# Kernel optimization log

Hardware: AMD Instinct MI355X
Metric: run time of the kernel (lower is better)

Reference implementation:

```python
import jax, jax.numpy as jnp
import numpy as np

B, S, D = 4, 2048, 1024
H = 16
HD = D // H  # head_dim = 64


def setup_inputs() -> dict:
    key = jax.random.key(0)
    ks = jax.random.split(key, 5)
    scale = 1.0 / np.sqrt(D)
    return {
        "x": jax.random.normal(ks[0], (B, S, D), dtype=jnp.float32),
        "Wq": jax.random.normal(ks[1], (D, D), dtype=jnp.float32) * scale,
        "Wk": jax.random.normal(ks[2], (D, D), dtype=jnp.float32) * scale,
        "Wv": jax.random.normal(ks[3], (D, D), dtype=jnp.float32) * scale,
        "Wo": jax.random.normal(ks[4], (D, D), dtype=jnp.float32) * scale,
        "bo": jnp.zeros((D,), dtype=jnp.float32),
    }


def reference(x, Wq, Wk, Wv, Wo, bo):
    b, s, d = x.shape
    # project and split heads: [b, h, s, hd]
    q = (x @ Wq).reshape(b, s, H, HD).transpose(0, 2, 1, 3)
    k = (x @ Wk).reshape(b, s, H, HD).transpose(0, 2, 1, 3)
    v = (x @ Wv).reshape(b, s, H, HD).transpose(0, 2, 1, 3)
    # scores: [b, h, s, s]
    scores = jnp.einsum("bhqd,bhkd->bhqk", q, k)
    # NOTE: original uses tril(diagonal=1) -> allows one future token (off-by-one)
    mask = jnp.tril(jnp.ones((s, s), dtype=bool), k=1)
    scores = jnp.where(mask, scores, -jnp.inf)
    attn = jax.nn.softmax(scores / np.sqrt(HD), axis=-1)
    # dropout p=0.0 (deterministic baseline): identity
    ctx = jnp.einsum("bhqk,bhkd->bhqd", attn, v)
    ctx = ctx.transpose(0, 2, 1, 3).reshape(b, s, d)
    return ctx @ Wo + bo
```

## Files before the change

### kernel.cpp

```cpp
#include <hip/hip_runtime.h>
#include <hip/hip_bf16.h>

#define Bq 4
#define Sq 2048
#define Dq 1024
#define Hq 16
#define HDq 64
#define Mq (Bq*Sq)

typedef unsigned short u16;
typedef __attribute__((ext_vector_type(8))) __bf16 b16x8;
typedef __attribute__((ext_vector_type(4))) float f32x4;
typedef __attribute__((ext_vector_type(4))) unsigned int u32x4;

__device__ inline float bf2f(u16 h){ union{unsigned u; float f;} v; v.u = ((unsigned)h)<<16; return v.f; }
__device__ inline u16 f2bf(float f){ union{float f; unsigned u;} v; v.f=f; unsigned r = v.u + 0x7FFFu + ((v.u>>16)&1u); return (u16)(r>>16); }
__device__ inline u16 truncbf(float f){ union{float f; unsigned u;} v; v.f=f; return (u16)(v.u>>16); }
__device__ inline float ld_elem(const void* p, size_t i, int isf32){
  return isf32 ? ((const float*)p)[i] : bf2f(((const u16*)p)[i]);
}
__device__ inline void ld16(const u16* g, u16* l){
  __builtin_amdgcn_global_load_lds((const __attribute__((address_space(1))) void*)g,
                                   (__attribute__((address_space(3))) void*)l, 16, 0, 0);
}

#if __has_builtin(__builtin_amdgcn_exp2f)
#define EXP2(x) __builtin_amdgcn_exp2f(x)
#else
#define EXP2(x) __expf((x)*0.69314718056f)
#endif
#define SCALE_LOG2E 0.18033688011112042f

__global__ void detect_dtype(const unsigned* __restrict__ x, int* __restrict__ flag){
  __shared__ int cnt;
  if(threadIdx.x==0) cnt=0;
  __syncthreads();
  int local=0;
  for(int i=threadIdx.x;i<2048;i+=256){
    unsigned w = x[i];
    if(((w>>7)&0xFFu)>=0x90u) local++;
    if(((w>>23)&0xFFu)>=0x90u) local++;
  }
  atomicAdd(&cnt, local);
  __syncthreads();
  if(threadIdx.x==0) *flag = (cnt>64) ? 1 : 0;
}

__global__ __launch_bounds__(256) void convert_x(const void* __restrict__ x, u16* __restrict__ xc,
                                                 const int* __restrict__ flag, int n){
  const int f = *flag;
  int i = (blockIdx.x*256 + threadIdx.x)*8;
  if(i>=n) return;
  if(f){
    const float* xf=(const float*)x;
    #pragma unroll
    for(int j=0;j<8;j++) xc[i+j] = f2bf(xf[i+j]);
  } else {
    *(u32x4*)&xc[i] = *(const u32x4*)((const u16*)x + i);
  }
}

__global__ __launch_bounds__(256) void transpose_w(
    const void* __restrict__ W0, const void* __restrict__ W1,
    const void* __restrict__ W2, const void* __restrict__ W3,
    u16* __restrict__ T0, u16* __restrict__ T1,
    u16* __restrict__ T2, u16* __restrict__ T3,
    const int* __restrict__ flag){
  __shared__ u16 tile[64][65];
  const int f = *flag;
  const int z = blockIdx.z;
  const void* src = (z==0)?W0:(z==1)?W1:(z==2)?W2:W3;
  u16*       dst = (z==0)?T0:(z==1)?T1:(z==2)?T2:T3;
  const int t = threadIdx.x;
  const int k0 = blockIdx.x*64, n0 = blockIdx.y*64;
  #pragma unroll
  for(int r=0;r<16;r++){
    int row = r*4 + (t>>6), col = t&63;
    tile[row][col] = f2bf(ld_elem(src, (size_t)(k0+row)*Dq + n0 + col, f));
  }
  __syncthreads();
  #pragma unroll
  for(int r=0;r<16;r++){
    int row = r*4 + (t>>6), col = t&63;
    dst[(size_t)(n0+row)*Dq + k0 + col] = tile[col][row];
  }
}

__global__ __launch_bounds__(256) void gemm_bf0(
    const u16* __restrict__ A, const u16* __restrict__ Bt,
    u16* __restrict__ O0, u16* __restrict__ O1, u16* __restrict__ O2){
  constexpr int NT = Dq/32;
  __shared__ u16 Apriv[2][4][2048];
  __shared__ u16 Bpriv[2][4][2048];
  const int t = threadIdx.x;
  const int lane = t & 63, wave = t >> 6;
  const int quad = lane >> 4, l16 = lane & 15;
  const int wr = wave >> 1, wc = wave & 1;
  int L = blockIdx.x + blockIdx.y*gridDim.x;
  int k8 = L & 7, ii = L >> 3;
  int nsb = ii >> 6, rem = ii & 63;
  int mg = rem >> 3, ng = rem & 7;
  const int m0 = (k8*8 + mg)*128, n0 = (nsb*8 + ng)*128;

  f32x4 acc[4][4] = {};

  auto stage = [&](int T, int s){
    const int k0 = T<<5;
    #pragma unroll
    for(int r=0;r<4;r++){
      int idx = lane + (r<<6);
      int row = idx>>2, g = idx&3;
      int gl = g ^ ((row>>1)&3);
      ld16(&A[(size_t)(m0 + wr*64 + row)*Dq + k0 + gl*8], &Apriv[s][wave][idx*8]);
    }
    #pragma unroll
    for(int r=0;r<4;r++){
      int idx = lane + (r<<6);
      int row = idx>>2, g = idx&3;
      int gl = g ^ ((row>>1)&3);
      ld16(&Bt[(size_t)(n0 + wc*64 + row)*Dq + k0 + gl*8], &Bpriv[s][wave][idx*8]);
    }
  };
  auto ldA = [&](int s, int i)->b16x8{
    int row = i*16 + l16;
    return *(const b16x8*)&Apriv[s][wave][row*32 + ((quad ^ ((row>>1)&3))<<3)];
  };
  auto ldB = [&](int s, int j)->b16x8{
    int row = j*16 + l16;
    return *(const b16x8*)&Bpriv[s][wave][row*32 + ((quad ^ ((row>>1)&3))<<3)];
  };
  #define MFMA_BF16 __builtin_amdgcn_mfma_f32_16x16x32_bf16

  stage(0, 0);

  for(int tt=0; tt<NT; ++tt){
    const int s = tt&1;
    if(tt+1<NT){
      stage(tt+1, s^1);
      asm volatile("s_waitcnt vmcnt(8)" ::: "memory");
    } else {
      asm volatile("s_waitcnt vmcnt(0)" ::: "memory");
    }
    __builtin_amdgcn_sched_barrier(0);
    b16x8 af[4], bf[4];
    #pragma unroll
    for(int i=0;i<4;i++) af[i]=ldA(s,i);
    #pragma unroll
    for(int j=0;j<4;j++) bf[j]=ldB(s,j);
    asm volatile("s_waitcnt lgkmcnt(0)" ::: "memory");
    __builtin_amdgcn_sched_barrier(0);
    __builtin_amdgcn_s_setprio(1);
    #pragma unroll
    for(int i=0;i<4;i++)
      #pragma unroll
      for(int j=0;j<4;j++)
        acc[i][j]=MFMA_BF16(af[i],bf[j],acc[i][j],0,0,0);
    __builtin_amdgcn_s_setprio(0);
  }

  #pragma unroll
  for(int i=0;i<4;i++){
    #pragma unroll
    for(int j=0;j<4;j++){
      int n = n0 + wc*64 + j*16 + l16;
      #pragma unroll
      for(int r=0;r<4;r++){
        int m = m0 + wr*64 + i*16 + quad*4 + r;
        float c = acc[i][j][r];
        int z = n >> 10, nn2 = n & 1023;
        int b = m >> 11, s2 = m & 2047;
        int h = nn2 >> 6, hd = nn2 & 63;
        if (z==0)      O0[(((size_t)(b*Hq + h))*Sq + s2)*HDq + hd] = f2bf(c*SCALE_LOG2E);
        else if (z==1) O1[(((size_t)(b*Hq + h))*Sq + s2)*HDq + hd] = f2bf(c);
        else           O2[(((size_t)(b*Hq + h))*HDq + hd)*Sq + s2] = f2bf(c);
      }
    }
  }
  #undef MFMA_BF16
}

__global__ __launch_bounds__(256, 3) void gemm_op(
    const u16* __restrict__ A, const u16* __restrict__ Bt,
    void* __restrict__ Og, const void* __restrict__ bias, const int* __restrict__ flag){
  constexpr int NT = Dq/32;
  __shared__ u16 Asl[3][128*32];
  __shared__ u16 Bsl[3][128*32];
  const int f = *flag;
  const int t = threadIdx.x;
  const int lane = t & 63, wave = t >> 6;
  const int quad = lane >> 4, l16 = lane & 15;
  const int wr = wave >> 1, wc = wave & 1;
  int L = blockIdx.x + blockIdx.y*gridDim.x;
  int k8 = L & 7, ii = L >> 3;
  int mg = ii >> 3, ng = ii & 7;
  const int m0 = (k8*8 + mg)*128, n0 = ng*128;

  f32x4 acc[4][4] = {};

  auto stageA = [&](int T, int s){
    #pragma unroll
    for(int r=0;r<2;r++){
      int idx = t + (r<<8);
      int row = idx>>2, g = idx&3;
      int gl = g ^ ((row>>1)&3);
      ld16(&A[(size_t)(m0+row)*Dq + (T<<5) + gl*8], &Asl[s][idx*8]);
    }
  };
  auto stageB = [&](int T, int s){
    #pragma unroll
    for(int r=0;r<2;r++){
      int idx = t + (r<<8);
      int row = idx>>2, g = idx&3;
      int gl = g ^ ((row>>1)&3);
      ld16(&Bt[(size_t)(n0+row)*Dq + (T<<5) + gl*8], &Bsl[s][idx*8]);
    }
  };
  auto ldA = [&](int s, int i)->b16x8{
    int row = wr*64 + i*16 + l16;
    return *(const b16x8*)&Asl[s][row*32 + ((quad ^ ((row>>1)&3))<<3)];
  };
  auto ldB = [&](int s, int j)->b16x8{
    int row = wc*64 + j*16 + l16;
    return *(const b16x8*)&Bsl[s][row*32 + ((quad ^ ((row>>1)&3))<<3)];
  };
  #define MFMA_BF16 __builtin_amdgcn_mfma_f32_16x16x32_bf16

  stageA(0,0); stageB(0,0); stageA(1,1); stageB(1,1);
  asm volatile("s_waitcnt vmcnt(4)" ::: "memory");
  __builtin_amdgcn_s_barrier();
  __builtin_amdgcn_sched_barrier(0);

  int s0=0, s1=1, s2=2;
  for(int tt=0; tt<NT; ++tt){
    if(tt+2<NT){ stageA(tt+2, s2); stageB(tt+2, s2); }
    b16x8 af[4], bf[4];
    #pragma unroll
    for(int i=0;i<4;i++) af[i]=ldA(s0,i);
    #pragma unroll
    for(int j=0;j<4;j++) bf[j]=ldB(s0,j);
    __builtin_amdgcn_s_barrier();
    asm volatile("s_waitcnt lgkmcnt(0)" ::: "memory");
    __builtin_amdgcn_sched_barrier(0);
    __builtin_amdgcn_s_setprio(1);
    #pragma unroll
    for(int i=0;i<4;i++)
      #pragma unroll
      for(int j=0;j<4;j++)
        acc[i][j]=MFMA_BF16(af[i],bf[j],acc[i][j],0,0,0);
    __builtin_amdgcn_s_setprio(0);
    if(tt<NT-2) asm volatile("s_waitcnt vmcnt(4)" ::: "memory");
    else        asm volatile("s_waitcnt vmcnt(0)" ::: "memory");
    __builtin_amdgcn_s_barrier();
    __builtin_amdgcn_sched_barrier(0);
    int x=s0; s0=s1; s1=s2; s2=x;
  }

  #pragma unroll
  for(int i=0;i<4;i++){
    #pragma unroll
    for(int j=0;j<4;j++){
      int n = n0 + wc*64 + j*16 + l16;
      #pragma unroll
      for(int r=0;r<4;r++){
        int m = m0 + wr*64 + i*16 + quad*4 + r;
        float c2 = acc[i][j][r] + ld_elem(bias, n, f);
        if (f) ((float*)Og)[(size_t)m*Dq + n] = c2;
        else   ((u16*)Og)[(size_t)m*Dq + n]   = f2bf(c2);
      }
    }
  }
  #undef MFMA_BF16
}

__global__ __launch_bounds__(256) void flash_attn(
    const u16* __restrict__ Q, const u16* __restrict__ K,
    const u16* __restrict__ VT, u16* __restrict__ C){
  __shared__ u16 Kt[128*64];
  __shared__ u16 Vt[64*128];
  __shared__ u16 Pl[4][16][72];
  const int t = threadIdx.x;
  const int lane = t&63, wave = t>>6, quad = lane>>4, l16 = lane&15;
  int L  = blockIdx.x + blockIdx.y*gridDim.x;
  int k8 = L & 7, ii = L >> 3;
  const int bh = k8*8 + (ii>>4);
  const int p  = ii & 15;
  const int b = bh >> 4, h = bh & 15;
  const int qt[2] = { p, 31 - p };
  int nk[2];
  #pragma unroll
  for(int tt=0;tt<2;tt++){ int v = qt[tt]+2; nk[tt] = (v<32)?v:32; }
  const int nrounds = (nk[1]+1)>>1;
  const u16* Qh = Q  + (size_t)bh*Sq*HDq;
  const u16* Kh = K  + (size_t)bh*Sq*HDq;
  const u16* Vh = VT + (size_t)bh*HDq*Sq;

  b16x8 aq[2][2];
  #pragma unroll
  for(int tt=0;tt<2;tt++){
    const u16* qp = Qh + (size_t)(qt[tt]*64 + wave*16 + l16)*HDq + quad*8;
    aq[tt][0] = *(const b16x8*)qp;
    aq[tt][1] = *(const b16x8*)(qp + 32);
  }
  b16x8 vone;
  #pragma unroll
  for(int i=0;i<8;i++) vone[i] = (__bf16)1.0f;

  const f32x4 fzero = {0.f,0.f,0.f,0.f};
  f32x4 Oa[2][4]; f32x4 lacc[2];
  #pragma unroll
  for(int tt=0;tt<2;tt++){ lacc[tt]=fzero; for(int j=0;j<4;j++) Oa[tt][j]=fzero; }

  for(int kt2=0; kt2<nrounds; kt2++){
    __syncthreads();
    #pragma unroll
    for(int r=0;r<4;r++){
      int idx = t + (r<<8);
      int row = idx>>3, g = idx&7;
      int csw = (g ^ (row&7))<<3;
      ld16(Kh + (size_t)(kt2*128+row)*HDq + csw, Kt + idx*8);
    }
    #pragma unroll
    for(int r=0;r<4;r++){
      int idx = t + (r<<8);
      int row = idx>>4, g = idx&15;
      int csw = (g ^ (row&15))<<3;
      ld16(Vh + (size_t)row*Sq + (size_t)kt2*128 + csw, Vt + idx*8);
    }
    __syncthreads();

    #pragma unroll
    for(int half=0; half<2; half++){
      const int kt = kt2*2 + half;
      #pragma unroll
      for(int tt=0;tt<2;tt++){
        if (kt >= nk[tt]) continue;
        const int qq0 = qt[tt]*64;
        f32x4 sc[4];
        #pragma unroll
        for(int jn=0;jn<4;jn++){
          int krow = half*64 + jn*16 + l16;
          const u16* kp = &Kt[krow*64];
          f32x4 s = fzero;
          b16x8 bk0 = *(const b16x8*)&kp[((quad     ^ (krow&7))<<3)];
          b16x8 bk1 = *(const b16x8*)&kp[(((quad+4) ^ (krow&7))<<3)];
          s = __builtin_amdgcn_mfma_f32_16x16x32_bf16(aq[tt][0], bk0, s, 0,0,0);
          s = __builtin_amdgcn_mfma_f32_16x16x32_bf16(aq[tt][1], bk1, s, 0,0,0);
          sc[jn] = s;
        }
        if (kt < qt[tt]) {
          #pragma unroll
          for(int jn=0;jn<4;jn++)
            #pragma unroll
            for(int r=0;r<4;r++)
              Pl[wave][quad*4+r][jn*16+l16] = truncbf(EXP2(sc[jn][r]));
        } else {
          const int qbase = qq0 + wave*16 + quad*4;
          #pragma unroll
          for(int jn=0;jn<4;jn++){
            int kg = kt*64 + jn*16 + l16;
            #pragma unroll
            for(int r=0;r<4;r++){
              float sv = sc[jn][r];
              if (kg > qbase + r + 1) sv = -__builtin_inff();
              Pl[wave][quad*4+r][jn*16+l16] = truncbf(EXP2(sv));
            }
          }
        }
        #pragma unroll
        for(int ks=0;ks<2;ks++){
          b16x8 ap = *(const b16x8*)&Pl[wave][l16][ks*32 + quad*8];
          int glog = half*8 + ks*4 + quad;
          #pragma unroll
          for(int jd=0;jd<4;jd++){
            int hd = jd*16 + l16;
            b16x8 bv = *(const b16x8*)&Vt[hd*128 + ((glog ^ (hd&15))<<3)];
            Oa[tt][jd] = __builtin_amdgcn_mfma_f32_16x16x32_bf16(ap, bv, Oa[tt][jd], 0,0,0);
          }
          lacc[tt] = __builtin_amdgcn_mfma_f32_16x16x32_bf16(ap, vone, lacc[tt], 0,0,0);
        }
      }
    }
  }
  #pragma unroll
  for(int tt=0;tt<2;tt++){
    const int qq0 = qt[tt]*64;
    #pragma unroll
    for(int r=0;r<4;r++){
      int s = qq0 + wave*16 + quad*4 + r;
      float inv = 1.0f / lacc[tt][r];
      #pragma unroll
      for(int jd=0;jd<4;jd++)
        C[((size_t)(b*Sq + s))*Dq + h*HDq + jd*16 + l16] = f2bf(Oa[tt][jd][r]*inv);
    }
  }
}

extern "C" void kernel_launch(void* const* d_in, const int* in_sizes, int n_in,
                              void* d_out, int out_size, void* d_ws, size_t ws_size,
                              hipStream_t stream){
  const void* x  = d_in[0];
  const void* Wq = d_in[1];
  const void* Wk = d_in[2];
  const void* Wv = d_in[3];
  const void* Wo = d_in[4];
  const void* bo = d_in[5];

  char* ws = (char*)d_ws;
  size_t off = 0;
  auto wsalloc = [&](size_t bytes)->void*{
    void* p = ws + off; off += (bytes + 255) & ~(size_t)255; return p;
  };
  int* flag = (int*)wsalloc(256);
  u16* WqT = (u16*)wsalloc((size_t)Dq*Dq*2);
  u16* WkT = (u16*)wsalloc((size_t)Dq*Dq*2);
  u16* WvT = (u16*)wsalloc((size_t)Dq*Dq*2);
  u16* WoT = (u16*)wsalloc((size_t)Dq*Dq*2);
  u16* xc  = (u16*)wsalloc((size_t)Mq*Dq*2);
  u16* Qb  = (u16*)wsalloc((size_t)Mq*Dq*2);
  u16* Kb  = (u16*)wsalloc((size_t)Mq*Dq*2);
  u16* VTb = (u16*)wsalloc((size_t)Mq*Dq*2);
  u16* Cb  = (u16*)wsalloc((size_t)Mq*Dq*2);

  detect_dtype<<<1, 256, 0, stream>>>((const unsigned*)x, flag);
  convert_x<<<dim3(Mq*Dq/8/256), 256, 0, stream>>>(x, xc, flag, Mq*Dq);
  transpose_w<<<dim3(16,16,4), 256, 0, stream>>>(Wq,Wk,Wv,Wo, WqT,WkT,WvT,WoT, flag);
  gemm_bf0<<<dim3(24, 64), 256, 0, stream>>>(xc, WqT, Qb,Kb,VTb);
  flash_attn<<<dim3(16, Bq*Hq), 256, 0, stream>>>(Qb, Kb, VTb, Cb);
  gemm_op<<<dim3(8, 64), 256, 0, stream>>>(Cb, WoT, d_out, bo, flag);
}
```

Before: 226.1 us.

## Fuse prep kernels with in-wave dtype detection; QKV GEMM loads A into registers

Merges dtype detection, x conversion and weight transposition into one prep kernel. Each wave now detects the dtype with a ballot over a sample of x, which removes the flag buffer and two launches. The QKV GEMM is restructured so A fragments are loaded straight from global memory into registers and double-buffered there, while B goes through a 3-stage shared LDS ring with barriers. The goal is less launch overhead and less LDS traffic, at the cost of uncoalesced direct A loads and extra block barriers.

```diff
diff --git a/kernel.cpp b/kernel.cpp
--- a/kernel.cpp
+++ b/kernel.cpp
@@ -31,67 +31,58 @@
 #endif
 #define SCALE_LOG2E 0.18033688011112042f
 
-__global__ void detect_dtype(const unsigned* __restrict__ x, int* __restrict__ flag){
-  __shared__ int cnt;
-  if(threadIdx.x==0) cnt=0;
-  __syncthreads();
-  int local=0;
-  for(int i=threadIdx.x;i<2048;i+=256){
-    unsigned w = x[i];
-    if(((w>>7)&0xFFu)>=0x90u) local++;
-    if(((w>>23)&0xFFu)>=0x90u) local++;
-  }
-  atomicAdd(&cnt, local);
-  __syncthreads();
-  if(threadIdx.x==0) *flag = (cnt>64) ? 1 : 0;
-}
-
-__global__ __launch_bounds__(256) void convert_x(const void* __restrict__ x, u16* __restrict__ xc,
-                                                 const int* __restrict__ flag, int n){
-  const int f = *flag;
-  int i = (blockIdx.x*256 + threadIdx.x)*8;
-  if(i>=n) return;
-  if(f){
-    const float* xf=(const float*)x;
-    #pragma unroll
-    for(int j=0;j<8;j++) xc[i+j] = f2bf(xf[i+j]);
-  } else {
-    *(u32x4*)&xc[i] = *(const u32x4*)((const u16*)x + i);
-  }
-}
-
-__global__ __launch_bounds__(256) void transpose_w(
+__device__ inline int detect_wave(const unsigned* __restrict__ x, int t){
+  unsigned w = x[t & 255];
+  unsigned long long m1 = __ballot(((w>>7)&0xFFu)>=0x90u);
+  unsigned long long m2 = __ballot(((w>>23)&0xFFu)>=0x90u);
+  return (__popcll(m1)+__popcll(m2)) > 8 ? 1 : 0;
+}
+
+__global__ __launch_bounds__(256) void prep(
+    const void* __restrict__ x,
     const void* __restrict__ W0, const void* __restrict__ W1,
     const void* __restrict__ W2, const void* __restrict__ W3,
+    u16* __restrict__ xc,
     u16* __restrict__ T0, u16* __restrict__ T1,
-    u16* __restrict__ T2, u16* __restrict__ T3,
-    const int* __restrict__ flag){
+    u16* __restrict__ T2, u16* __restrict__ T3){
   __shared__ u16 tile[64][65];
-  const int f = *flag;
-  const int z = blockIdx.z;
-  const void* src = (z==0)?W0:(z==1)?W1:(z==2)?W2:W3;
-  u16*       dst = (z==0)?T0:(z==1)?T1:(z==2)?T2:T3;
   const int t = threadIdx.x;
-  const int k0 = blockIdx.x*64, n0 = blockIdx.y*64;
-  #pragma unroll
-  for(int r=0;r<16;r++){
-    int row = r*4 + (t>>6), col = t&63;
-    tile[row][col] = f2bf(ld_elem(src, (size_t)(k0+row)*Dq + n0 + col, f));
-  }
-  __syncthreads();
-  #pragma unroll
-  for(int r=0;r<16;r++){
-    int row = r*4 + (t>>6), col = t&63;
-    dst[(size_t)(n0+row)*Dq + k0 + col] = tile[col][row];
-  }
-}
-
-__global__ __launch_bounds__(256) void gemm_bf0(
+  const int f = detect_wave((const unsigned*)x, t);
+  const int bid = blockIdx.x;
+  if (bid < 4096){
+    int i = (bid*256 + t)*8;
+    if(f){
+      const float* xf=(const float*)x;
+      #pragma unroll
+      for(int j=0;j<8;j++) xc[i+j] = f2bf(xf[i+j]);
+    } else {
+      *(u32x4*)&xc[i] = *(const u32x4*)((const u16*)x + i);
+    }
+  } else {
+    int idx = bid - 4096;
+    int z = idx >> 8, rem = idx & 255;
+    int k0 = (rem & 15)*64, n0 = (rem >> 4)*64;
+    const void* src = (z==0)?W0:(z==1)?W1:(z==2)?W2:W3;
+    u16*       dst = (z==0)?T0:(z==1)?T1:(z==2)?T2:T3;
+    #pragma unroll
+    for(int r=0;r<16;r++){
+      int row = r*4 + (t>>6), col = t&63;
+      tile[row][col] = f2bf(ld_elem(src, (size_t)(k0+row)*Dq + n0 + col, f));
+    }
+    __syncthreads();
+    #pragma unroll
+    for(int r=0;r<16;r++){
+      int row = r*4 + (t>>6), col = t&63;
+      dst[(size_t)(n0+row)*Dq + k0 + col] = tile[col][row];
+    }
+  }
+}
+
+__global__ __launch_bounds__(256) void gemm_ar(
     const u16* __restrict__ A, const u16* __restrict__ Bt,
     u16* __restrict__ O0, u16* __restrict__ O1, u16* __restrict__ O2){
   constexpr int NT = Dq/32;
-  __shared__ u16 Apriv[2][4][2048];
-  __shared__ u16 Bpriv[2][4][2048];
+  __shared__ u16 Bsl[3][128*32];
   const int t = threadIdx.x;
   const int lane = t & 63, wave = t >> 6;
   const int quad = lane >> 4, l16 = lane & 15;
@@ -103,50 +94,48 @@
   const int m0 = (k8*8 + mg)*128, n0 = (nsb*8 + ng)*128;
 
   f32x4 acc[4][4] = {};
-
-  auto stage = [&](int T, int s){
-    const int k0 = T<<5;
-    #pragma unroll
-    for(int r=0;r<4;r++){
-      int idx = lane + (r<<6);
+  const u16* Arow = A + (size_t)(m0 + wr*64 + l16)*Dq + quad*8;
+
+  auto loadA = [&](int T, b16x8 (&d)[4]){
+    #pragma unroll
+    for(int i=0;i<4;i++)
+      d[i] = *(const b16x8*)(Arow + (size_t)(i*16)*Dq + (T<<5));
+  };
+  auto stageB = [&](int T, int s){
+    #pragma unroll
+    for(int r=0;r<2;r++){
+      int idx = t + (r<<8);
       int row = idx>>2, g = idx&3;
       int gl = g ^ ((row>>1)&3);
-      ld16(&A[(size_t)(m0 + wr*64 + row)*Dq + k0 + gl*8], &Apriv[s][wave][idx*8]);
-    }
-    #pragma unroll
-    for(int r=0;r<4;r++){
-      int idx = lane + (r<<6);
-      int row = idx>>2, g = idx&3;
-      int gl = g ^ ((row>>1)&3);
-      ld16(&Bt[(size_t)(n0 + wc*64 + row)*Dq + k0 + gl*8], &Bpriv[s][wave][idx*8]);
-    }
-  };
-  auto ldA = [&](int s, int i)->b16x8{
-    int row = i*16 + l16;
-    return *(const b16x8*)&Apriv[s][wave][row*32 + ((quad ^ ((row>>1)&3))<<3)];
+      ld16(&Bt[(size_t)(n0+row)*Dq + (T<<5) + gl*8], &Bsl[s][idx*8]);
+    }
   };
   auto ldB = [&](int s, int j)->b16x8{
-    int row = j*16 + l16;
-    return *(const b16x8*)&Bpriv[s][wave][row*32 + ((quad ^ ((row>>1)&3))<<3)];
+    int row = wc*64 + j*16 + l16;
+    return *(const b16x8*)&Bsl[s][row*32 + ((quad ^ ((row>>1)&3))<<3)];
   };
   #define MFMA_BF16 __builtin_amdgcn_mfma_f32_16x16x32_bf16
 
-  stage(0, 0);
-
-  for(int tt=0; tt<NT; ++tt){
-    const int s = tt&1;
-    if(tt+1<NT){
-      stage(tt+1, s^1);
-      asm volatile("s_waitcnt vmcnt(8)" ::: "memory");
-    } else {
-      asm volatile("s_waitcnt vmcnt(0)" ::: "memory");
-    }
+  b16x8 aA[4], aB[4];
+  int s0=0, s1=1, s2=2;
+
+  loadA(0, aA);
+  stageB(0,0); stageB(1,1);
+  asm volatile("s_waitcnt vmcnt(2)" ::: "memory");
+  __builtin_amdgcn_s_barrier();
+  __builtin_amdgcn_sched_barrier(0);
+
+  auto step = [&](int tt, b16x8 (&cur)[4], b16x8 (&nxt)[4]){
+    if(tt+1<NT) loadA(tt+1, nxt);
+    if(tt+2<NT) stageB(tt+2, s2);
+    if(tt+2<NT)      asm volatile("s_waitcnt vmcnt(8)" ::: "memory");
+    else if(tt+1<NT) asm volatile("s_waitcnt vmcnt(6)" ::: "memory");
+    else             asm volatile("s_waitcnt vmcnt(0)" ::: "memory");
+    __builtin_amdgcn_s_barrier();
     __builtin_amdgcn_sched_barrier(0);
-    b16x8 af[4], bf[4];
-    #pragma unroll
-    for(int i=0;i<4;i++) af[i]=ldA(s,i);
-    #pragma unroll
-    for(int j=0;j<4;j++) bf[j]=ldB(s,j);
+    b16x8 bf[4];
+    #pragma unroll
+    for(int j=0;j<4;j++) bf[j]=ldB(s0,j);
     asm volatile("s_waitcnt lgkmcnt(0)" ::: "memory");
     __builtin_amdgcn_sched_barrier(0);
     __builtin_amdgcn_s_setprio(1);
@@ -154,9 +143,13 @@
     for(int i=0;i<4;i++)
       #pragma unroll
       for(int j=0;j<4;j++)
-        acc[i][j]=MFMA_BF16(af[i],bf[j],acc[i][j],0,0,0);
+        acc[i][j]=MFMA_BF16(cur[i],bf[j],acc[i][j],0,0,0);
     __builtin_amdgcn_s_setprio(0);
-  }
+    __builtin_amdgcn_s_barrier();
+    __builtin_amdgcn_sched_barrier(0);
+    int x2=s0; s0=s1; s1=s2; s2=x2;
+  };
+  for(int t2=0; t2<NT; t2+=2){ step(t2, aA, aB); step(t2+1, aB, aA); }
 
   #pragma unroll
   for(int i=0;i<4;i++){
@@ -168,11 +161,11 @@
         int m = m0 + wr*64 + i*16 + quad*4 + r;
         float c = acc[i][j][r];
         int z = n >> 10, nn2 = n & 1023;
-        int b = m >> 11, s2 = m & 2047;
+        int b = m >> 11, s2x = m & 2047;
         int h = nn2 >> 6, hd = nn2 & 63;
-        if (z==0)      O0[(((size_t)(b*Hq + h))*Sq + s2)*HDq + hd] = f2bf(c*SCALE_LOG2E);
-        else if (z==1) O1[(((size_t)(b*Hq + h))*Sq + s2)*HDq + hd] = f2bf(c);
-        else           O2[(((size_t)(b*Hq + h))*HDq + hd)*Sq + s2] = f2bf(c);
+        if (z==0)      O0[(((size_t)(b*Hq + h))*Sq + s2x)*HDq + hd] = f2bf(c*SCALE_LOG2E);
+        else if (z==1) O1[(((size_t)(b*Hq + h))*Sq + s2x)*HDq + hd] = f2bf(c);
+        else           O2[(((size_t)(b*Hq + h))*HDq + hd)*Sq + s2x] = f2bf(c);
       }
     }
   }
@@ -181,11 +174,12 @@
 
 __global__ __launch_bounds__(256, 3) void gemm_op(
     const u16* __restrict__ A, const u16* __restrict__ Bt,
-    void* __restrict__ Og, const void* __restrict__ bias, const int* __restrict__ flag){
+    void* __restrict__ Og, const void* __restrict__ bias,
+    const unsigned* __restrict__ xdet){
+  const int f = detect_wave(xdet, threadIdx.x);
   constexpr int NT = Dq/32;
   __shared__ u16 Asl[3][128*32];
   __shared__ u16 Bsl[3][128*32];
-  const int f = *flag;
   const int t = threadIdx.x;
   const int lane = t & 63, wave = t >> 6;
   const int quad = lane >> 4, l16 = lane & 15;
@@ -252,7 +246,7 @@
     else        asm volatile("s_waitcnt vmcnt(0)" ::: "memory");
     __builtin_amdgcn_s_barrier();
     __builtin_amdgcn_sched_barrier(0);
-    int x=s0; s0=s1; s1=s2; s2=x;
+    int x2=s0; s0=s1; s1=s2; s2=x2;
   }
 
   #pragma unroll
@@ -410,7 +404,6 @@
   auto wsalloc = [&](size_t bytes)->void*{
     void* p = ws + off; off += (bytes + 255) & ~(size_t)255; return p;
   };
-  int* flag = (int*)wsalloc(256);
   u16* WqT = (u16*)wsalloc((size_t)Dq*Dq*2);
   u16* WkT = (u16*)wsalloc((size_t)Dq*Dq*2);
   u16* WvT = (u16*)wsalloc((size_t)Dq*Dq*2);
@@ -421,10 +414,8 @@
   u16* VTb = (u16*)wsalloc((size_t)Mq*Dq*2);
   u16* Cb  = (u16*)wsalloc((size_t)Mq*Dq*2);
 
-  detect_dtype<<<1, 256, 0, stream>>>((const unsigned*)x, flag);
-  convert_x<<<dim3(Mq*Dq/8/256), 256, 0, stream>>>(x, xc, flag, Mq*Dq);
-  transpose_w<<<dim3(16,16,4), 256, 0, stream>>>(Wq,Wk,Wv,Wo, WqT,WkT,WvT,WoT, flag);
-  gemm_bf0<<<dim3(24, 64), 256, 0, stream>>>(xc, WqT, Qb,Kb,VTb);
+  prep<<<dim3(5120), 256, 0, stream>>>(x, Wq,Wk,Wv,Wo, xc, WqT,WkT,WvT,WoT);
+  gemm_ar<<<dim3(24, 64), 256, 0, stream>>>(xc, WqT, Qb,Kb,VTb);
   flash_attn<<<dim3(16, Bq*Hq), 256, 0, stream>>>(Qb, Kb, VTb, Cb);
-  gemm_op<<<dim3(8, 64), 256, 0, stream>>>(Cb, WoT, d_out, bo, flag);
-}
+  gemm_op<<<dim3(8, 64), 256, 0, stream>>>(Cb, WoT, d_out, bo, (const unsigned*)x);
+}
```

Measured after the change: 245.1 us. +8.4%, slower.
